# Performance work log

Measured on AMD Instinct MI355X. Metric: run time of the kernel, lower is better.

## Reference

```python
import jax, jax.numpy as jnp
import numpy as np

B, S, H = 2, 2048, 768
NH, HD = 12, 64  # num heads, head dim


def setup_inputs() -> dict:
    key = jax.random.key(0)
    ks = jax.random.split(key, 9)
    std = 0.02
    def dense(k):
        return jax.random.normal(k, (H, H), dtype=jnp.float32) * std
    return {
        "hidden_states": jax.random.normal(ks[0], (B, S, H), dtype=jnp.float32),
        "attention_mask": jnp.ones((B, S), dtype=jnp.int32),
        "Wq": dense(ks[1]), "bq": jnp.zeros((H,), jnp.float32),
        "Wk": dense(ks[2]), "bk": jnp.zeros((H,), jnp.float32),
        "Wv": dense(ks[3]), "bv": jnp.zeros((H,), jnp.float32),
        "Wo": dense(ks[4]), "bo": jnp.zeros((H,), jnp.float32),
    }


def reference(hidden_states, attention_mask, Wq, bq, Wk, bk, Wv, bv, Wo, bo):
    # QKV projections -> [B, NH, S, HD]
    def split_heads(x):
        return x.reshape(B, S, NH, HD).transpose(0, 2, 1, 3)
    q = split_heads(hidden_states @ Wq + bq)
    k = split_heads(hidden_states @ Wk + bk)
    v = split_heads(hidden_states @ Wv + bv)
    # scaled dot-product scores [B, NH, S, S]
    scores = jnp.einsum('bhqd,bhkd->bhqk', q, k) / jnp.sqrt(jnp.float32(HD))
    adder = (1.0 - attention_mask.astype(jnp.float32)) * -10000.0
    scores = scores + adder[:, None, None, :]
    probs = jax.nn.softmax(scores, axis=-1)
    # dropout is identity at inference
    ctx = jnp.einsum('bhqk,bhkd->bhqd', probs, v)
    ctx = ctx.transpose(0, 2, 1, 3).reshape(B, S, H)
    return ctx @ Wo + bo
```

## Files before the change

### kernel.cpp

```cpp
#include <hip/hip_runtime.h>
#include <hip/hip_bf16.h>

#define DI __device__ __forceinline__

using bf16x8 = __attribute__((ext_vector_type(8))) short;
using f32x4  = __attribute__((ext_vector_type(4))) float;
using f32x16 = __attribute__((ext_vector_type(16))) float;
using u16    = unsigned short;
using u16x4  = __attribute__((ext_vector_type(4))) unsigned short;

constexpr int Bc = 2, Sc = 2048, Hc = 768, NHc = 12, HDc = 64;
constexpr int Mc = Bc * Sc;
constexpr float L2E = 1.4426950408889634f;

DI u16 f2bf(float f) {
  union { float f; unsigned u; } c; c.f = f;
  unsigned u = c.u;
  return (u16)((u + 0x7fffu + ((u >> 16) & 1u)) >> 16);
}

DI unsigned f2bf2(float a, float b) {
  float2 t; t.x = a; t.y = b;
  __hip_bfloat162 h = __float22bfloat162_rn(t);
  union { __hip_bfloat162 h; unsigned u; } c; c.h = h;
  return c.u;
}

DI void gload_lds16(const void* g, void* l) {
  __builtin_amdgcn_global_load_lds(
      (__attribute__((address_space(1))) void*)(g),
      (__attribute__((address_space(3))) void*)(l), 16, 0, 0);
}


__global__ void cvt_bf16(const float* __restrict__ x, u16* __restrict__ y, int n4,
                         const int* __restrict__ maskg, u16* __restrict__ mones) {
  int i = blockIdx.x * 256 + threadIdx.x;
  if (i >= n4) return;
  float4 v = reinterpret_cast<const float4*>(x)[i];
  u16x4 o;
  o[0] = f2bf(v.x); o[1] = f2bf(v.y); o[2] = f2bf(v.z); o[3] = f2bf(v.w);
  reinterpret_cast<u16x4*>(y)[i] = o;
  if (i < Bc * Sc / 4) {
    int j = i & 3;
    int js = ((j & 1) << 1) | ((j >> 1) & 1);
    int isrc = (i & ~3) | js;
    int4 mv = reinterpret_cast<const int4*>(maskg)[isrc];
    u16x4 m;
    m[0] = f2bf((float)mv.x); m[1] = f2bf((float)mv.y);
    m[2] = f2bf((float)mv.z); m[3] = f2bf((float)mv.w);
    reinterpret_cast<u16x4*>(mones)[i] = m;
  }
}

__global__ void wtrans(const float* __restrict__ Wq, const float* __restrict__ Wk,
                       const float* __restrict__ Wv, const float* __restrict__ Wo,
                       u16* __restrict__ Tq, u16* __restrict__ Tk,
                       u16* __restrict__ Tv, u16* __restrict__ To) {
  __shared__ float tile[32][33];
  const float* W; u16* T;
  switch (blockIdx.z) {
    case 0:  W = Wq; T = Tq; break;
    case 1:  W = Wk; T = Tk; break;
    case 2:  W = Wv; T = Tv; break;
    default: W = Wo; T = To; break;
  }
  int tx = threadIdx.x, ty = threadIdx.y;
  int n0 = blockIdx.x * 32, k0 = blockIdx.y * 32;
#pragma unroll
  for (int j = 0; j < 4; ++j) tile[ty + j * 8][tx] = W[(k0 + ty + j * 8) * Hc + n0 + tx];
  __syncthreads();
#pragma unroll
  for (int j = 0; j < 4; ++j) T[(n0 + ty + j * 8) * Hc + k0 + tx] = f2bf(tile[tx][ty + j * 8]);
}


DI void gemm_core(const u16* __restrict__ Ag, const u16* __restrict__ Btg,
                  u16* Asm, u16* Bsm, int m0, int n0,
                  int tid, int lane, int wr, int wc, f32x4 acc[4][4]) {
  const int lo = lane & 15, hi = lane >> 4;
  const int r1 = tid >> 2, c1 = tid & 3;
  for (int kt = 0; kt < Hc / 32; ++kt) {
    const int k0 = kt * 32;
    {
      int row = r1, cg = c1 ^ ((row >> 1) & 3);
      gload_lds16(Ag  + (size_t)(row + m0) * Hc + k0 + cg * 8, Asm + tid * 8);
      gload_lds16(Btg + (size_t)(row + n0) * Hc + k0 + cg * 8, Bsm + tid * 8);
      row = r1 + 64; cg = c1 ^ ((row >> 1) & 3);
      gload_lds16(Ag  + (size_t)(row + m0) * Hc + k0 + cg * 8, Asm + (tid + 256) * 8);
      gload_lds16(Btg + (size_t)(row + n0) * Hc + k0 + cg * 8, Bsm + (tid + 256) * 8);
    }
    __syncthreads();
    bf16x8 af[4], bf[4];
#pragma unroll
    for (int m = 0; m < 4; ++m) {
      int rowa = wr * 64 + m * 16 + lo;
      af[m] = *reinterpret_cast<const bf16x8*>(Asm + rowa * 32 + ((hi ^ ((rowa >> 1) & 3)) * 8));
      int rowb = wc * 64 + m * 16 + lo;
      bf[m] = *reinterpret_cast<const bf16x8*>(Bsm + rowb * 32 + ((hi ^ ((rowb >> 1) & 3)) * 8));
    }
#pragma unroll
    for (int m = 0; m < 4; ++m)
#pragma unroll
      for (int n = 0; n < 4; ++n)
        acc[m][n] = __builtin_amdgcn_mfma_f32_16x16x32_bf16(af[m], bf[n], acc[m][n], 0, 0, 0);
    __syncthreads();
  }
}


__launch_bounds__(256)
__global__ void qkv_gemm(const u16* __restrict__ Xb,
                         const u16* __restrict__ Wtq, const u16* __restrict__ Wtk,
                         const u16* __restrict__ Wtv,
                         const float* __restrict__ bq, const float* __restrict__ bk,
                         const float* __restrict__ bv, const int* __restrict__ maskg,
                         u16* __restrict__ Qo, u16* __restrict__ Ko, u16* __restrict__ Vto) {
  __shared__ __attribute__((aligned(16))) u16 Asm[128 * 32];
  __shared__ __attribute__((aligned(16))) u16 Bsm[128 * 32];
  const int tid = threadIdx.x, lane = tid & 63, w = tid >> 6;
  const int wr = w >> 1, wc = w & 1;
  const int m0 = blockIdx.x * 128, n0 = blockIdx.y * 128;
  const int z = blockIdx.z;
  const u16* Bt = (z == 0) ? Wtq : ((z == 1) ? Wtk : Wtv);
  const float* bias = (z == 0) ? bq : ((z == 1) ? bk : bv);
  f32x4 acc[4][4] = {};
  gemm_core(Xb, Bt, Asm, Bsm, m0, n0, tid, lane, wr, wc, acc);
  const int lo = lane & 15, hi = lane >> 4;
  const float scl = (z == 0) ? 0.125f * L2E : 1.0f;
#pragma unroll
  for (int m = 0; m < 4; ++m)
#pragma unroll
    for (int n = 0; n < 4; ++n)
#pragma unroll
      for (int r = 0; r < 4; ++r) {
        int gm = m0 + wr * 64 + m * 16 + hi * 4 + r;
        int gn = n0 + wc * 64 + n * 16 + lo;
        float v = (acc[m][n][r] + bias[gn]) * scl;
        int b = gm >> 11, s = gm & 2047, h = gn >> 6, d = gn & 63;
        if (z == 2) {
          v *= (float)maskg[b * Sc + s];
          int sp = (s & ~12) | ((s & 4) << 1) | ((s & 8) >> 1);
          Vto[((b * NHc + h) * HDc + d) * Sc + sp] = f2bf(v);
        } else {
          int idx = (((b * NHc + h) * Sc) + s) * HDc + d;
          if (z == 0) Qo[idx] = f2bf(v); else Ko[idx] = f2bf(v);
        }
      }
}


__launch_bounds__(256)
__global__ void out_gemm(const u16* __restrict__ Ctx, const u16* __restrict__ Wto,
                         const float* __restrict__ bo, float* __restrict__ out) {
  __shared__ __attribute__((aligned(16))) u16 Asm[128 * 32];
  __shared__ __attribute__((aligned(16))) u16 Bsm[128 * 32];
  const int tid = threadIdx.x, lane = tid & 63, w = tid >> 6;
  const int wr = w >> 1, wc = w & 1;
  const int m0 = blockIdx.x * 128, n0 = blockIdx.y * 128;
  f32x4 acc[4][4] = {};
  gemm_core(Ctx, Wto, Asm, Bsm, m0, n0, tid, lane, wr, wc, acc);
  const int lo = lane & 15, hi = lane >> 4;
#pragma unroll
  for (int m = 0; m < 4; ++m)
#pragma unroll
    for (int n = 0; n < 4; ++n)
#pragma unroll
      for (int r = 0; r < 4; ++r) {
        int gm = m0 + wr * 64 + m * 16 + hi * 4 + r;
        int gn = n0 + wc * 64 + n * 16 + lo;
        out[(size_t)gm * Hc + gn] = acc[m][n][r] + bo[gn];
      }
}


DI bf16x8 lds_rd(const u16* base, int row, int c8) {
  return *reinterpret_cast<const bf16x8*>(base + row * 64 + ((c8 ^ (row & 7)) << 3));
}

DI float vmax16(const f32x16& v) {
  float a0 = fmaxf(v[0], v[8]),  a1 = fmaxf(v[1], v[9]);
  float a2 = fmaxf(v[2], v[10]), a3 = fmaxf(v[3], v[11]);
  float a4 = fmaxf(v[4], v[12]), a5 = fmaxf(v[5], v[13]);
  float a6 = fmaxf(v[6], v[14]), a7 = fmaxf(v[7], v[15]);
  float b0 = fmaxf(a0, a4), b1 = fmaxf(a1, a5);
  float b2 = fmaxf(a2, a6), b3 = fmaxf(a3, a7);
  return fmaxf(fmaxf(b0, b1), fmaxf(b2, b3));
}

DI bf16x8 pkfrag0(const f32x16& p) {
  union { unsigned u[4]; bf16x8 v; } a;
  a.u[0] = f2bf2(p[0], p[1]); a.u[1] = f2bf2(p[2], p[3]);
  a.u[2] = f2bf2(p[4], p[5]); a.u[3] = f2bf2(p[6], p[7]);
  return a.v;
}
DI bf16x8 pkfrag1(const f32x16& p) {
  union { unsigned u[4]; bf16x8 v; } a;
  a.u[0] = f2bf2(p[8], p[9]);   a.u[1] = f2bf2(p[10], p[11]);
  a.u[2] = f2bf2(p[12], p[13]); a.u[3] = f2bf2(p[14], p[15]);
  return a.v;
}

__launch_bounds__(128)
__global__ void attn(const u16* __restrict__ Qg, const u16* __restrict__ Kg,
                     const u16* __restrict__ Vtg, const u16* __restrict__ monesG,
                     u16* __restrict__ ctxg) {
  __shared__ __attribute__((aligned(16))) u16 Ksm[3][64 * 64];
  __shared__ __attribute__((aligned(16))) u16 Vsm[3][64 * 64];
  __shared__ __attribute__((aligned(16))) u16 Mo[Sc];

  const int tid = threadIdx.x, lane = tid & 63, w = tid >> 6;
  const int l31 = lane & 31, hi2 = lane >> 5;

  const int id = blockIdx.x;
  const int xcd = id & 7, sub = id >> 3;
  const int head = xcd * 3 + (sub >> 5);
  const int q0 = (sub & 31) * 64;
  const int b = head / NHc, h = head % NHc;

  const u16* Qh = Qg + (size_t)head * Sc * HDc;
  const u16* Kh = Kg + (size_t)head * Sc * HDc;
  const u16* Vh = Vtg + (size_t)head * HDc * Sc;

#pragma unroll
  for (int j = 0; j < 2; ++j) {
    int ch = tid + j * 128;
    gload_lds16(monesG + (size_t)b * Sc + ch * 8, Mo + ch * 8);
  }

  const int qglob = q0 + w * 32 + l31;
  bf16x8 qf[4];
#pragma unroll
  for (int c = 0; c < 4; ++c)
    qf[c] = *reinterpret_cast<const bf16x8*>(Qh + (size_t)qglob * HDc + c * 16 + hi2 * 8);

  __syncthreads();

  u16 *K0 = &Ksm[0][0], *K1 = &Ksm[1][0], *K2 = &Ksm[2][0];
  u16 *V0 = &Vsm[0][0], *V1 = &Vsm[1][0], *V2 = &Vsm[2][0];

  auto stage = [&](u16* Kd, u16* Vd, int kv0) {
#pragma unroll
    for (int j = 0; j < 4; ++j) {
      int ch = tid + j * 128;
      int row = ch >> 3, cg = (ch & 7) ^ (row & 7);
      gload_lds16(Kh + (size_t)(kv0 + row) * HDc + cg * 8, Kd + ch * 8);
    }
#pragma unroll
    for (int j = 0; j < 4; ++j) {
      int ch = tid + j * 128;
      int row = ch >> 3, cg = (ch & 7) ^ (row & 7);
      gload_lds16(Vh + (size_t)row * Sc + kv0 + cg * 8, Vd + ch * 8);
    }
  };

  stage(K0, V0, 0);
  stage(K1, V1, 64);

  f32x16 oacc0 = {}, oacc1 = {}, lacc = {};
  float mrow = -1e30f;

  constexpr int NT = Sc / 64;
  for (int t = 0; t < NT; ++t) {
    __builtin_amdgcn_sched_barrier(0);
    __builtin_amdgcn_s_barrier();
    __builtin_amdgcn_sched_barrier(0);
    if (t + 2 < NT) {
      stage(K2, V2, (t + 2) * 64);
      asm volatile("s_waitcnt vmcnt(16)" ::: "memory");
    } else if (t + 2 == NT) {
      asm volatile("s_waitcnt vmcnt(8)" ::: "memory");
    } else {
      asm volatile("s_waitcnt vmcnt(0)" ::: "memory");
    }
    __builtin_amdgcn_sched_barrier(0);
    __builtin_amdgcn_s_barrier();
    __builtin_amdgcn_sched_barrier(0);

    const u16* Ks = K0;
    const u16* Vs = V0;

    f32x16 s0 = {}, s1 = {};
    __builtin_amdgcn_s_setprio(1);
#pragma unroll
    for (int c = 0; c < 4; ++c) {
      bf16x8 kf0 = lds_rd(Ks, l31, 2 * c + hi2);
      bf16x8 kf1 = lds_rd(Ks, 32 + l31, 2 * c + hi2);
      s0 = __builtin_amdgcn_mfma_f32_32x32x16_bf16(kf0, qf[c], s0, 0, 0, 0);
      s1 = __builtin_amdgcn_mfma_f32_32x32x16_bf16(kf1, qf[c], s1, 0, 0, 0);
    }
    __builtin_amdgcn_s_setprio(0);

    float pmax = fmaxf(vmax16(s0), vmax16(s1));
    pmax = fmaxf(pmax, __shfl_xor(pmax, 32, 64));
    if (!__all(pmax - mrow <= 8.0f)) {
      float nm = fmaxf(mrow, pmax);
      float sc = exp2f(mrow - nm);
      mrow = nm;
#pragma unroll
      for (int rr = 0; rr < 16; ++rr) {
        int qi = (rr & 3) + 8 * (rr >> 2) + 4 * hi2;
        float sb = __shfl(sc, qi, 64);
        oacc0[rr] *= sb; oacc1[rr] *= sb; lacc[rr] *= sb;
      }
    }
#pragma unroll
    for (int j = 0; j < 16; ++j) s0[j] = exp2f(s0[j] - mrow);
#pragma unroll
    for (int j = 0; j < 16; ++j) s1[j] = exp2f(s1[j] - mrow);

    bf16x8 paf[4];
    paf[0] = pkfrag0(s0);
    paf[1] = pkfrag1(s0);
    paf[2] = pkfrag0(s1);
    paf[3] = pkfrag1(s1);

    __builtin_amdgcn_s_setprio(1);
#pragma unroll
    for (int c4 = 0; c4 < 4; ++c4) {
      bf16x8 mo = *reinterpret_cast<const bf16x8*>(Mo + t * 64 + c4 * 16 + hi2 * 8);
      bf16x8 vf0 = lds_rd(Vs, l31, 2 * c4 + hi2);
      bf16x8 vf1 = lds_rd(Vs, 32 + l31, 2 * c4 + hi2);
      lacc  = __builtin_amdgcn_mfma_f32_32x32x16_bf16(paf[c4], mo, lacc, 0, 0, 0);
      oacc0 = __builtin_amdgcn_mfma_f32_32x32x16_bf16(paf[c4], vf0, oacc0, 0, 0, 0);
      oacc1 = __builtin_amdgcn_mfma_f32_32x32x16_bf16(paf[c4], vf1, oacc1, 0, 0, 0);
    }
    __builtin_amdgcn_s_setprio(0);

    u16* tk = K0; K0 = K1; K1 = K2; K2 = tk;
    u16* tv = V0; V0 = V1; V1 = V2; V2 = tv;
  }

#pragma unroll
  for (int rr = 0; rr < 16; ++rr) {
    float inv = 1.0f / lacc[rr];
    int qi = (rr & 3) + 8 * (rr >> 2) + 4 * hi2;
    int s = q0 + w * 32 + qi;
    size_t base = (size_t)(b * Sc + s) * Hc + h * HDc;
    ctxg[base + l31]      = f2bf(oacc0[rr] * inv);
    ctxg[base + 32 + l31] = f2bf(oacc1[rr] * inv);
  }
}


extern "C" void kernel_launch(void* const* d_in, const int* in_sizes, int n_in,
                              void* d_out, int out_size, void* d_ws, size_t ws_size,
                              hipStream_t stream) {
  const float* hs  = (const float*)d_in[0];
  const int* mask  = (const int*)d_in[1];
  const float* Wq  = (const float*)d_in[2];
  const float* bq  = (const float*)d_in[3];
  const float* Wk  = (const float*)d_in[4];
  const float* bk  = (const float*)d_in[5];
  const float* Wv  = (const float*)d_in[6];
  const float* bv  = (const float*)d_in[7];
  const float* Wo  = (const float*)d_in[8];
  const float* bo  = (const float*)d_in[9];

  char* ws = (char*)d_ws;
  u16* Xb  = (u16*)(ws);
  u16* Wtq = (u16*)(ws + 6291456);
  u16* Wtk = Wtq + 589824;
  u16* Wtv = Wtk + 589824;
  u16* Wto = Wtv + 589824;
  u16* Qb  = (u16*)(ws + 11010048);
  u16* Kb  = Qb + 3145728;
  u16* Vtb = Kb + 3145728;
  u16* Ctx = Vtb + 3145728;
  u16* Mns = Ctx + 3145728;

  cvt_bf16<<<(Mc * Hc / 4 + 255) / 256, 256, 0, stream>>>(hs, Xb, Mc * Hc / 4, mask, Mns);
  wtrans<<<dim3(24, 24, 4), dim3(32, 8), 0, stream>>>(Wq, Wk, Wv, Wo, Wtq, Wtk, Wtv, Wto);
  qkv_gemm<<<dim3(32, 6, 3), 256, 0, stream>>>(Xb, Wtq, Wtk, Wtv, bq, bk, bv, mask, Qb, Kb, Vtb);
  attn<<<768, 128, 0, stream>>>(Qb, Kb, Vtb, Mns, Ctx);
  out_gemm<<<dim3(32, 6), 256, 0, stream>>>(Ctx, Wto, bo, (float*)d_out);
}
```

Before: 149.1 us.

## Split attention along KV into two halves with a separate combine kernel

Adds a split-KV (flash-decoding style) attention path. Each block handles half of the key/value sequence using 32-wide KV tiles, which doubles the grid from 768 to 1536 blocks. Each block writes unnormalised fp32 partial outputs, row sums and maxima, and a new combine kernel merges the two halves into the bf16 context. This is meant to raise occupancy and CU utilisation, at the cost of extra fp32 partial traffic, an extra launch and smaller MFMA tiles per iteration. The split path runs only when the workspace is large enough; otherwise the original kernel is used.

New measurement: 159.3 us, median of 2. +6.8%, slower.

```diff
diff --git a/kernel.cpp b/kernel.cpp
--- a/kernel.cpp
+++ b/kernel.cpp
@@ -177,6 +177,9 @@
 DI bf16x8 lds_rd(const u16* base, int row, int c8) {
   return *reinterpret_cast<const bf16x8*>(base + row * 64 + ((c8 ^ (row & 7)) << 3));
 }
+DI bf16x8 lds_rd4(const u16* base, int row, int c4) {
+  return *reinterpret_cast<const bf16x8*>(base + row * 32 + ((c4 ^ (row & 3)) << 3));
+}
 
 DI float vmax16(const f32x16& v) {
   float a0 = fmaxf(v[0], v[8]),  a1 = fmaxf(v[1], v[9]);
@@ -201,23 +204,26 @@
   return a.v;
 }
 
+#define ATTN_BAR()  do { __builtin_amdgcn_sched_barrier(0); \
+                         __builtin_amdgcn_s_barrier();      \
+                         __builtin_amdgcn_sched_barrier(0); } while (0)
+
+
 __launch_bounds__(128)
-__global__ void attn(const u16* __restrict__ Qg, const u16* __restrict__ Kg,
-                     const u16* __restrict__ Vtg, const u16* __restrict__ monesG,
-                     u16* __restrict__ ctxg) {
+__global__ void attn_full(const u16* __restrict__ Qg, const u16* __restrict__ Kg,
+                          const u16* __restrict__ Vtg, const u16* __restrict__ monesG,
+                          u16* __restrict__ ctxg) {
   __shared__ __attribute__((aligned(16))) u16 Ksm[3][64 * 64];
   __shared__ __attribute__((aligned(16))) u16 Vsm[3][64 * 64];
   __shared__ __attribute__((aligned(16))) u16 Mo[Sc];
 
   const int tid = threadIdx.x, lane = tid & 63, w = tid >> 6;
   const int l31 = lane & 31, hi2 = lane >> 5;
-
   const int id = blockIdx.x;
   const int xcd = id & 7, sub = id >> 3;
   const int head = xcd * 3 + (sub >> 5);
   const int q0 = (sub & 31) * 64;
   const int b = head / NHc, h = head % NHc;
-
   const u16* Qh = Qg + (size_t)head * Sc * HDc;
   const u16* Kh = Kg + (size_t)head * Sc * HDc;
   const u16* Vh = Vtg + (size_t)head * HDc * Sc;
@@ -227,18 +233,15 @@
     int ch = tid + j * 128;
     gload_lds16(monesG + (size_t)b * Sc + ch * 8, Mo + ch * 8);
   }
-
   const int qglob = q0 + w * 32 + l31;
   bf16x8 qf[4];
 #pragma unroll
   for (int c = 0; c < 4; ++c)
     qf[c] = *reinterpret_cast<const bf16x8*>(Qh + (size_t)qglob * HDc + c * 16 + hi2 * 8);
-
   __syncthreads();
 
   u16 *K0 = &Ksm[0][0], *K1 = &Ksm[1][0], *K2 = &Ksm[2][0];
   u16 *V0 = &Vsm[0][0], *V1 = &Vsm[1][0], *V2 = &Vsm[2][0];
-
   auto stage = [&](u16* Kd, u16* Vd, int kv0) {
 #pragma unroll
     for (int j = 0; j < 4; ++j) {
@@ -253,18 +256,14 @@
       gload_lds16(Vh + (size_t)row * Sc + kv0 + cg * 8, Vd + ch * 8);
     }
   };
-
   stage(K0, V0, 0);
   stage(K1, V1, 64);
 
   f32x16 oacc0 = {}, oacc1 = {}, lacc = {};
   float mrow = -1e30f;
-
   constexpr int NT = Sc / 64;
   for (int t = 0; t < NT; ++t) {
-    __builtin_amdgcn_sched_barrier(0);
-    __builtin_amdgcn_s_barrier();
-    __builtin_amdgcn_sched_barrier(0);
+    ATTN_BAR();
     if (t + 2 < NT) {
       stage(K2, V2, (t + 2) * 64);
       asm volatile("s_waitcnt vmcnt(16)" ::: "memory");
@@ -273,13 +272,9 @@
     } else {
       asm volatile("s_waitcnt vmcnt(0)" ::: "memory");
     }
-    __builtin_amdgcn_sched_barrier(0);
-    __builtin_amdgcn_s_barrier();
-    __builtin_amdgcn_sched_barrier(0);
-
+    ATTN_BAR();
     const u16* Ks = K0;
     const u16* Vs = V0;
-
     f32x16 s0 = {}, s1 = {};
     __builtin_amdgcn_s_setprio(1);
 #pragma unroll
@@ -290,7 +285,6 @@
       s1 = __builtin_amdgcn_mfma_f32_32x32x16_bf16(kf1, qf[c], s1, 0, 0, 0);
     }
     __builtin_amdgcn_s_setprio(0);
-
     float pmax = fmaxf(vmax16(s0), vmax16(s1));
     pmax = fmaxf(pmax, __shfl_xor(pmax, 32, 64));
     if (!__all(pmax - mrow <= 8.0f)) {
@@ -308,13 +302,9 @@
     for (int j = 0; j < 16; ++j) s0[j] = exp2f(s0[j] - mrow);
 #pragma unroll
     for (int j = 0; j < 16; ++j) s1[j] = exp2f(s1[j] - mrow);
-
     bf16x8 paf[4];
-    paf[0] = pkfrag0(s0);
-    paf[1] = pkfrag1(s0);
-    paf[2] = pkfrag0(s1);
-    paf[3] = pkfrag1(s1);
-
+    paf[0] = pkfrag0(s0); paf[1] = pkfrag1(s0);
+    paf[2] = pkfrag0(s1); paf[3] = pkfrag1(s1);
     __builtin_amdgcn_s_setprio(1);
 #pragma unroll
     for (int c4 = 0; c4 < 4; ++c4) {
@@ -326,11 +316,9 @@
       oacc1 = __builtin_amdgcn_mfma_f32_32x32x16_bf16(paf[c4], vf1, oacc1, 0, 0, 0);
     }
     __builtin_amdgcn_s_setprio(0);
-
     u16* tk = K0; K0 = K1; K1 = K2; K2 = tk;
     u16* tv = V0; V0 = V1; V1 = V2; V2 = tv;
   }
-
 #pragma unroll
   for (int rr = 0; rr < 16; ++rr) {
     float inv = 1.0f / lacc[rr];
@@ -340,6 +328,166 @@
     ctxg[base + l31]      = f2bf(oacc0[rr] * inv);
     ctxg[base + 32 + l31] = f2bf(oacc1[rr] * inv);
   }
+}
+
+
+__launch_bounds__(128)
+__global__ void attn_split(const u16* __restrict__ Qg, const u16* __restrict__ Kg,
+                           const u16* __restrict__ Vtg, const u16* __restrict__ monesG,
+                           float* __restrict__ Po, float* __restrict__ Pl,
+                           float* __restrict__ Pm) {
+  __shared__ __attribute__((aligned(16))) u16 Ksm[3][32 * 64];
+  __shared__ __attribute__((aligned(16))) u16 Vsm[3][64 * 32];
+  __shared__ __attribute__((aligned(16))) u16 Mo[1024];
+
+  const int tid = threadIdx.x, lane = tid & 63, w = tid >> 6;
+  const int l31 = lane & 31, hi2 = lane >> 5;
+  const int id = blockIdx.x;
+  const int xcd = id & 7, sub = id >> 3;
+  const int head = xcd * 3 + (sub >> 6);
+  const int r = sub & 63;
+  const int q0 = (r >> 1) * 64;
+  const int kh = r & 1;
+  const int b = head / NHc;
+  const int kvbase = kh * 1024;
+
+  const u16* Qh = Qg + (size_t)head * Sc * HDc;
+  const u16* Kh = Kg + (size_t)head * Sc * HDc;
+  const u16* Vh = Vtg + (size_t)head * HDc * Sc;
+
+  gload_lds16(monesG + (size_t)b * Sc + kvbase + tid * 8, Mo + tid * 8);
+
+  const int qglob = q0 + w * 32 + l31;
+  bf16x8 qf[4];
+#pragma unroll
+  for (int c = 0; c < 4; ++c)
+    qf[c] = *reinterpret_cast<const bf16x8*>(Qh + (size_t)qglob * HDc + c * 16 + hi2 * 8);
+  __syncthreads();
+
+  u16 *K0 = &Ksm[0][0], *K1 = &Ksm[1][0], *K2 = &Ksm[2][0];
+  u16 *V0 = &Vsm[0][0], *V1 = &Vsm[1][0], *V2 = &Vsm[2][0];
+
+  auto stage = [&](u16* Kd, u16* Vd, int kv0) {
+#pragma unroll
+    for (int j = 0; j < 2; ++j) {
+      int ch = tid + j * 128;
+      int row = ch >> 3, cg = (ch & 7) ^ (row & 7);
+      gload_lds16(Kh + (size_t)(kv0 + row) * HDc + cg * 8, Kd + ch * 8);
+    }
+#pragma unroll
+    for (int j = 0; j < 2; ++j) {
+      int ch = tid + j * 128;
+      int row = ch >> 2, cg = (ch & 3) ^ (row & 3);
+      gload_lds16(Vh + (size_t)row * Sc + kv0 + cg * 8, Vd + ch * 8);
+    }
+  };
+  stage(K0, V0, kvbase);
+  stage(K1, V1, kvbase + 32);
+
+  f32x16 oacc0 = {}, oacc1 = {}, lacc = {};
+  float mrow = -1e30f;
+  constexpr int NT = 32;
+  for (int t = 0; t < NT; ++t) {
+    ATTN_BAR();
+    if (t + 2 < NT) {
+      stage(K2, V2, kvbase + (t + 2) * 32);
+      asm volatile("s_waitcnt vmcnt(8)" ::: "memory");
+    } else if (t + 2 == NT) {
+      asm volatile("s_waitcnt vmcnt(4)" ::: "memory");
+    } else {
+      asm volatile("s_waitcnt vmcnt(0)" ::: "memory");
+    }
+    ATTN_BAR();
+    const u16* Ks = K0;
+    const u16* Vs = V0;
+
+    f32x16 s0 = {};
+    __builtin_amdgcn_s_setprio(1);
+#pragma unroll
+    for (int c = 0; c < 4; ++c) {
+      bf16x8 kf = lds_rd(Ks, l31, 2 * c + hi2);
+      s0 = __builtin_amdgcn_mfma_f32_32x32x16_bf16(kf, qf[c], s0, 0, 0, 0);
+    }
+    __builtin_amdgcn_s_setprio(0);
+
+    float pmax = vmax16(s0);
+    pmax = fmaxf(pmax, __shfl_xor(pmax, 32, 64));
+    if (!__all(pmax - mrow <= 8.0f)) {
+      float nm = fmaxf(mrow, pmax);
+      float sc = exp2f(mrow - nm);
+      mrow = nm;
+#pragma unroll
+      for (int rr = 0; rr < 16; ++rr) {
+        int qi = (rr & 3) + 8 * (rr >> 2) + 4 * hi2;
+        float sb = __shfl(sc, qi, 64);
+        oacc0[rr] *= sb; oacc1[rr] *= sb; lacc[rr] *= sb;
+      }
+    }
+#pragma unroll
+    for (int j = 0; j < 16; ++j) s0[j] = exp2f(s0[j] - mrow);
+
+    bf16x8 paf0 = pkfrag0(s0), paf1 = pkfrag1(s0);
+
+    __builtin_amdgcn_s_setprio(1);
+#pragma unroll
+    for (int c4 = 0; c4 < 2; ++c4) {
+      bf16x8 pa = c4 ? paf1 : paf0;
+      bf16x8 mo = *reinterpret_cast<const bf16x8*>(Mo + t * 32 + c4 * 16 + hi2 * 8);
+      bf16x8 vf0 = lds_rd4(Vs, l31, 2 * c4 + hi2);
+      bf16x8 vf1 = lds_rd4(Vs, 32 + l31, 2 * c4 + hi2);
+      lacc  = __builtin_amdgcn_mfma_f32_32x32x16_bf16(pa, mo, lacc, 0, 0, 0);
+      oacc0 = __builtin_amdgcn_mfma_f32_32x32x16_bf16(pa, vf0, oacc0, 0, 0, 0);
+      oacc1 = __builtin_amdgcn_mfma_f32_32x32x16_bf16(pa, vf1, oacc1, 0, 0, 0);
+    }
+    __builtin_amdgcn_s_setprio(0);
+
+    u16* tk = K0; K0 = K1; K1 = K2; K2 = tk;
+    u16* tv = V0; V0 = V1; V1 = V2; V2 = tv;
+  }
+
+  const size_t pbase = ((size_t)(kh * 24 + head)) * Sc;
+#pragma unroll
+  for (int rr = 0; rr < 16; ++rr) {
+    int qi = (rr & 3) + 8 * (rr >> 2) + 4 * hi2;
+    int q = q0 + w * 32 + qi;
+    float* dst = Po + (pbase + q) * HDc;
+    dst[l31]      = oacc0[rr];
+    dst[32 + l31] = oacc1[rr];
+  }
+  if (l31 == 0) {
+#pragma unroll
+    for (int rr = 0; rr < 16; ++rr) {
+      int qi = (rr & 3) + 8 * (rr >> 2) + 4 * hi2;
+      Pl[pbase + q0 + w * 32 + qi] = lacc[rr];
+    }
+  }
+  if (hi2 == 0) Pm[pbase + q0 + w * 32 + l31] = mrow;
+}
+
+
+__global__ void combine(const float* __restrict__ Po, const float* __restrict__ Pl,
+                        const float* __restrict__ Pm, u16* __restrict__ ctxg) {
+  int idx = blockIdx.x * 256 + threadIdx.x;
+  int head = idx >> 15;
+  int rem = idx & 32767;
+  int q = rem >> 4, d4 = rem & 15;
+  size_t hq = (size_t)head * Sc + q;
+  const size_t HSTR = (size_t)24 * Sc;
+  float m0 = Pm[hq], m1 = Pm[HSTR + hq];
+  float l0 = Pl[hq], l1 = Pl[HSTR + hq];
+  float M = fmaxf(m0, m1);
+  float e0 = exp2f(m0 - M), e1 = exp2f(m1 - M);
+  float inv = 1.0f / (l0 * e0 + l1 * e1);
+  const float4* P4 = reinterpret_cast<const float4*>(Po);
+  float4 o0 = P4[hq * 16 + d4];
+  float4 o1 = P4[(HSTR + hq) * 16 + d4];
+  u16x4 pk;
+  pk[0] = f2bf((o0.x * e0 + o1.x * e1) * inv);
+  pk[1] = f2bf((o0.y * e0 + o1.y * e1) * inv);
+  pk[2] = f2bf((o0.z * e0 + o1.z * e1) * inv);
+  pk[3] = f2bf((o0.w * e0 + o1.w * e1) * inv);
+  int b = head / NHc, h = head - b * NHc;
+  *reinterpret_cast<u16x4*>(ctxg + (size_t)(b * Sc + q) * Hc + h * HDc + d4 * 4) = pk;
 }
 
 
@@ -368,10 +516,19 @@
   u16* Vtb = Kb + 3145728;
   u16* Ctx = Vtb + 3145728;
   u16* Mns = Ctx + 3145728;
+  float* Po = (float*)(ws + 36184064);
+  float* Pl = (float*)(ws + 61349888);
+  float* Pm = (float*)(ws + 61743104);
+  const bool use_split = ws_size >= 62136320ull;
 
   cvt_bf16<<<(Mc * Hc / 4 + 255) / 256, 256, 0, stream>>>(hs, Xb, Mc * Hc / 4, mask, Mns);
   wtrans<<<dim3(24, 24, 4), dim3(32, 8), 0, stream>>>(Wq, Wk, Wv, Wo, Wtq, Wtk, Wtv, Wto);
   qkv_gemm<<<dim3(32, 6, 3), 256, 0, stream>>>(Xb, Wtq, Wtk, Wtv, bq, bk, bv, mask, Qb, Kb, Vtb);
-  attn<<<768, 128, 0, stream>>>(Qb, Kb, Vtb, Mns, Ctx);
+  if (use_split) {
+    attn_split<<<1536, 128, 0, stream>>>(Qb, Kb, Vtb, Mns, Po, Pl, Pm);
+    combine<<<3072, 256, 0, stream>>>(Po, Pl, Pm, Ctx);
+  } else {
+    attn_full<<<768, 128, 0, stream>>>(Qb, Kb, Vtb, Mns, Ctx);
+  }
   out_gemm<<<dim3(32, 6), 256, 0, stream>>>(Ctx, Wto, bo, (float*)d_out);
 }
```
